# Kernel tuning notes

Measured on AMD Instinct MI355X. Metric: run time of the kernel, lower is better.

The kernel has to match this reference:

```python
import jax, jax.numpy as jnp
import numpy as np

V = 4          # view_num
B = 2048       # batch_size
D = 512        # feature dim
N = V * B
TEMP = 0.5     # temperature
EPS = 1e-8     # torch CosineSimilarity eps


def _neg_idx():
    # Row with residue p (position within its view block) masks out columns c
    # with c % B == p (the positive/self positions), exactly matching
    # mask_positive_samples: fill_diagonal_(0) on every BxB block.
    cols = np.arange(N)
    return np.stack([cols[cols % B != p] for p in range(B)])  # [B, N-V]

_NEG_IDX = jnp.asarray(_neg_idx())


def setup_inputs() -> dict:
    key = jax.random.key(0)
    x = jax.random.normal(key, (V, B, D), dtype=jnp.float32)
    return {"x": x}


def reference(x):
    # torch.cat(input, dim=0) -> [N, D]
    xf = x.reshape(N, D)
    # Cosine similarity via normalize + matmul (same math as broadcasted
    # CosineSimilarity(dim=2), expressed efficiently).
    norm = jnp.maximum(jnp.linalg.norm(xf, axis=1, keepdims=True), EPS)
    xn = xf / norm
    sim = (xn @ xn.T) / TEMP                                  # [N, N]

    # Negatives per anchor row: gather masked columns (same column order as
    # torch boolean-mask indexing, which is row-major ascending).
    sim_v = sim.reshape(V, B, N)
    negs = jnp.take_along_axis(sim_v, _NEG_IDX[None], axis=2)  # [V, B, N-V]
    lse_neg = jax.nn.logsumexp(negs, axis=2)                   # [V, B]

    # pos[i, j, b] = sim block-diagonal between views i and j
    pos = jnp.diagonal(sim.reshape(V, B, V, B), axis1=1, axis2=3)  # [V, V, B]

    # CrossEntropy with label 0 on logits = [pos_ij, negatives_i]:
    #   loss_b = logsumexp([pos, negs]) - pos = logaddexp(pos, lse_neg) - pos
    lse = jnp.logaddexp(pos, lse_neg[:, None, :])              # [V, V, B]
    per_pair = (lse - pos).sum(axis=2) / B                     # [V, V]

    off_diag = 1.0 - jnp.eye(V, dtype=per_pair.dtype)          # skip j == i
    return jnp.sum(per_pair * off_diag)
```

## Files before the change

kernel.cpp:

```cpp
#include <hip/hip_runtime.h>
#include <hip/hip_fp8.h>

#define NV 4
#define NB 2048
#define ND 512
#define NN 8192

typedef int int8v __attribute__((ext_vector_type(8)));
typedef int int4v __attribute__((ext_vector_type(4)));
typedef float floatx4 __attribute__((ext_vector_type(4)));
#define SCALE1 0x7F7F7F7Fu

__global__ __launch_bounds__(256) void normalize_k(const float* __restrict__ x,
                                                   unsigned char* __restrict__ xn,
                                                   float* __restrict__ sumexp,
                                                   float* __restrict__ out) {
  if (threadIdx.x < 4) sumexp[blockIdx.x * 4 + threadIdx.x] = 0.0f;
  if (blockIdx.x == 0 && threadIdx.x == 0) out[0] = 0.0f;

  const int row = blockIdx.x * 4 + (threadIdx.x >> 6);
  const int l = threadIdx.x & 63;
  const float4* xr = (const float4*)(x + (size_t)row * ND);
  float4 v0 = xr[l * 2 + 0];
  float4 v1 = xr[l * 2 + 1];
  float ss = v0.x * v0.x + v0.y * v0.y + v0.z * v0.z + v0.w * v0.w +
             v1.x * v1.x + v1.y * v1.y + v1.z * v1.z + v1.w * v1.w;
#pragma unroll
  for (int off = 32; off > 0; off >>= 1) ss += __shfl_xor(ss, off, 64);
  const float inv = 1.0f / fmaxf(sqrtf(ss), 1e-8f);
  union { unsigned char b[8]; uint2 u; } pk;
  pk.b[0] = __hip_fp8_e4m3(v0.x * inv).__x;
  pk.b[1] = __hip_fp8_e4m3(v0.y * inv).__x;
  pk.b[2] = __hip_fp8_e4m3(v0.z * inv).__x;
  pk.b[3] = __hip_fp8_e4m3(v0.w * inv).__x;
  pk.b[4] = __hip_fp8_e4m3(v1.x * inv).__x;
  pk.b[5] = __hip_fp8_e4m3(v1.y * inv).__x;
  pk.b[6] = __hip_fp8_e4m3(v1.z * inv).__x;
  pk.b[7] = __hip_fp8_e4m3(v1.w * inv).__x;
  *(uint2*)(xn + (size_t)row * ND + l * 8) = pk.u;
}

__global__ __launch_bounds__(512, 2) void sim_k(const unsigned char* __restrict__ xn,
                                                float* __restrict__ sumexp,
                                                float* __restrict__ pos) {
  __shared__ unsigned char As[2 * 256 * 128];
  __shared__ unsigned char Bs[2 * 256 * 128];
  const int tid = threadIdx.x;
  const int l = tid & 63;
  const int m = l & 15, q = l >> 4, s = l & 7;
  const int wid = tid >> 6;
  const int wr = wid >> 2, wc = wid & 3;

  const int bid = blockIdx.x;
  int rt = (int)((65.0f - sqrtf(4225.0f - 8.0f * (float)bid)) * 0.5f);
  rt = rt < 0 ? 0 : (rt > 31 ? 31 : rt);
  while (rt > 0 && (rt * (65 - rt) / 2) > bid) --rt;
  while (rt < 31 && ((rt + 1) * (64 - rt) / 2) <= bid) ++rt;
  const int ct = rt + (bid - rt * (65 - rt) / 2);
  const bool diag = (rt == ct);

  floatx4 acc[8][4] = {};

  const unsigned char* gA = xn + (size_t)rt * 256 * ND;
  const unsigned char* gB = xn + (size_t)ct * 256 * ND;

  const int crow = tid >> 3;
  const int coff = (tid & 7) * 16;
  const int lsw = ((tid & 7) ^ ((tid >> 3) & 7)) * 16;

  const int fo0 = ((2 * q + 0) ^ s) * 16;
  const int fo1 = ((2 * q + 1) ^ s) * 16;

  int4v pA[4], pB[4];
#pragma unroll
  for (int i = 0; i < 4; ++i) {
    const size_t go = (size_t)(i * 64 + crow) * ND + coff;
    pA[i] = *(const int4v*)(gA + go);
    pB[i] = *(const int4v*)(gB + go);
  }

#pragma unroll 1
  for (int kt = 0; kt < 4; ++kt) {
    unsigned char* Ab = As + (kt & 1) * (256 * 128);
    unsigned char* Bb = Bs + (kt & 1) * (256 * 128);
#pragma unroll
    for (int i = 0; i < 4; ++i) {
      const int la = (i * 64 + crow) * 128 + lsw;
      *(int4v*)(Ab + la) = pA[i];
      *(int4v*)(Bb + la) = pB[i];
    }
    __syncthreads();
    if (kt < 3) {
      const int kb = (kt + 1) * 128;
#pragma unroll
      for (int i = 0; i < 4; ++i) {
        const size_t go = (size_t)(i * 64 + crow) * ND + kb + coff;
        pA[i] = *(const int4v*)(gA + go);
        pB[i] = *(const int4v*)(gB + go);
      }
    }
    int8v bf0, bf1, bf2, bf3;
    {
      const unsigned char* pb0 = Bb + (wc * 64 + 0 * 16 + m) * 128;
      const unsigned char* pb1 = Bb + (wc * 64 + 1 * 16 + m) * 128;
      const unsigned char* pb2 = Bb + (wc * 64 + 2 * 16 + m) * 128;
      const unsigned char* pb3 = Bb + (wc * 64 + 3 * 16 + m) * 128;
      bf0 = __builtin_shufflevector(*(const int4v*)(pb0 + fo0),
                                    *(const int4v*)(pb0 + fo1), 0,1,2,3,4,5,6,7);
      bf1 = __builtin_shufflevector(*(const int4v*)(pb1 + fo0),
                                    *(const int4v*)(pb1 + fo1), 0,1,2,3,4,5,6,7);
      bf2 = __builtin_shufflevector(*(const int4v*)(pb2 + fo0),
                                    *(const int4v*)(pb2 + fo1), 0,1,2,3,4,5,6,7);
      bf3 = __builtin_shufflevector(*(const int4v*)(pb3 + fo0),
                                    *(const int4v*)(pb3 + fo1), 0,1,2,3,4,5,6,7);
    }
    __builtin_amdgcn_s_setprio(1);
#pragma unroll
    for (int mt = 0; mt < 8; ++mt) {
      const unsigned char* pa = Ab + (wr * 128 + mt * 16 + m) * 128;
      const int8v af = __builtin_shufflevector(*(const int4v*)(pa + fo0),
                                               *(const int4v*)(pa + fo1),
                                               0,1,2,3,4,5,6,7);
      acc[mt][0] = __builtin_amdgcn_mfma_scale_f32_16x16x128_f8f6f4(
          af, bf0, acc[mt][0], 0, 0, 0, SCALE1, 0, SCALE1);
      acc[mt][1] = __builtin_amdgcn_mfma_scale_f32_16x16x128_f8f6f4(
          af, bf1, acc[mt][1], 0, 0, 0, SCALE1, 0, SCALE1);
      acc[mt][2] = __builtin_amdgcn_mfma_scale_f32_16x16x128_f8f6f4(
          af, bf2, acc[mt][2], 0, 0, 0, SCALE1, 0, SCALE1);
      acc[mt][3] = __builtin_amdgcn_mfma_scale_f32_16x16x128_f8f6f4(
          af, bf3, acc[mt][3], 0, 0, 0, SCALE1, 0, SCALE1);
    }
    __builtin_amdgcn_s_setprio(0);
  }

  const int r0 = rt * 256 + wr * 128;
  const int c0 = ct * 256 + wc * 64;
  float cs[4] = {0.f, 0.f, 0.f, 0.f};
#pragma unroll
  for (int mt = 0; mt < 8; ++mt) {
    float rs[4] = {0.f, 0.f, 0.f, 0.f};
#pragma unroll
    for (int nt = 0; nt < 4; ++nt) {
      const int c = c0 + nt * 16 + m;
#pragma unroll
      for (int reg = 0; reg < 4; ++reg) {
        const int r = r0 + mt * 16 + q * 4 + reg;
        const float sv = acc[mt][nt][reg] * 2.0f;
        if (((c - r) & (NB - 1)) == 0) {
          pos[r * NV + (c >> 11)] = sv;
          if (!diag) pos[c * NV + (r >> 11)] = sv;
        } else {
          const float e = __expf(sv);
          rs[reg] += e;
          cs[nt] += e;
        }
      }
    }
#pragma unroll
    for (int off = 1; off < 16; off <<= 1) {
#pragma unroll
      for (int reg = 0; reg < 4; ++reg) rs[reg] += __shfl_xor(rs[reg], off, 64);
    }
    if (m < 4) atomicAdd(&sumexp[r0 + mt * 16 + q * 4 + m], rs[m]);
  }
  if (!diag) {
#pragma unroll
    for (int nt = 0; nt < 4; ++nt) {
      cs[nt] += __shfl_xor(cs[nt], 16, 64);
      cs[nt] += __shfl_xor(cs[nt], 32, 64);
    }
    if (q == 0) {
#pragma unroll
      for (int nt = 0; nt < 4; ++nt)
        atomicAdd(&sumexp[c0 + nt * 16 + m], cs[nt]);
    }
  }
}

__global__ __launch_bounds__(256) void finalize_k(
    const float* __restrict__ sumexp, const float* __restrict__ pos,
    float* __restrict__ out) {
  const int r = blockIdx.x * 256 + threadIdx.x;
  const float se = sumexp[r];
  const int i = r >> 11;
  float local = 0.0f;
#pragma unroll
  for (int j = 0; j < NV; ++j) {
    if (j == i) continue;
    const float p = pos[r * NV + j];
    local += logf(__expf(p) + se) - p;
  }
  local *= (1.0f / NB);
#pragma unroll
  for (int off = 32; off > 0; off >>= 1) local += __shfl_xor(local, off, 64);
  if ((threadIdx.x & 63) == 0) atomicAdd(out, local);
}

extern "C" void kernel_launch(void* const* d_in, const int* in_sizes, int n_in,
                              void* d_out, int out_size, void* d_ws,
                              size_t ws_size, hipStream_t stream) {
  const float* x = (const float*)d_in[0];
  float* out = (float*)d_out;
  char* ws = (char*)d_ws;
  unsigned char* xn = (unsigned char*)ws;
  float* sumexp = (float*)(ws + (size_t)NN * ND);
  float* pos = (float*)(ws + (size_t)NN * ND + NN * 4);

  normalize_k<<<NN / 4, 256, 0, stream>>>(x, xn, sumexp, out);
  sim_k<<<32 * 33 / 2, 512, 0, stream>>>(xn, sumexp, pos);
  finalize_k<<<NN / 256, 256, 0, stream>>>(sumexp, pos, out);
}
```

Measured before the change: 113.2 us.

## Stream tiles with direct global-to-LDS loads in a split-phase MFMA pipeline

Replaces the register-staged global loads and LDS stores with global_load_lds DMA into swizzled shared memory. Each K step is split into two half-tile MFMA phases, and loads for later stages are issued between them under explicit vmcnt/lgkmcnt waits and raw barriers. It also remaps block IDs so consecutive blocks spread across the triangular tile order, which may help L2 locality across XCDs. The intent is to free VGPRs and overlap memory traffic with compute. The cost is fragile manual synchronization: the slot reuse of A half 0 for stage t+2 relies on exact wait counts.

```diff
diff --git a/kernel.cpp b/kernel.cpp
--- a/kernel.cpp
+++ b/kernel.cpp
@@ -43,15 +43,19 @@
 __global__ __launch_bounds__(512, 2) void sim_k(const unsigned char* __restrict__ xn,
                                                 float* __restrict__ sumexp,
                                                 float* __restrict__ pos) {
-  __shared__ unsigned char As[2 * 256 * 128];
-  __shared__ unsigned char Bs[2 * 256 * 128];
+#define TS (256 * 128)
+  __shared__ unsigned char As[2 * TS];
+  __shared__ unsigned char Bs[2 * TS];
   const int tid = threadIdx.x;
   const int l = tid & 63;
   const int m = l & 15, q = l >> 4, s = l & 7;
-  const int wid = tid >> 6;
-  const int wr = wid >> 2, wc = wid & 3;
-
-  const int bid = blockIdx.x;
+  const int w = tid >> 6;
+  const int wr = w >> 2, wc = w & 3;
+  const int w8 = w * 8;
+  const int l8 = l >> 3;
+  const int csw = ((l & 7) ^ l8) * 16;
+
+  const int bid = (blockIdx.x & 7) * 66 + (blockIdx.x >> 3);
   int rt = (int)((65.0f - sqrtf(4225.0f - 8.0f * (float)bid)) * 0.5f);
   rt = rt < 0 ? 0 : (rt > 31 ? 31 : rt);
   while (rt > 0 && (rt * (65 - rt) / 2) > bid) --rt;
@@ -64,73 +68,101 @@
   const unsigned char* gA = xn + (size_t)rt * 256 * ND;
   const unsigned char* gB = xn + (size_t)ct * 256 * ND;
 
-  const int crow = tid >> 3;
-  const int coff = (tid & 7) * 16;
-  const int lsw = ((tid & 7) ^ ((tid >> 3) & 7)) * 16;
-
   const int fo0 = ((2 * q + 0) ^ s) * 16;
   const int fo1 = ((2 * q + 1) ^ s) * 16;
 
-  int4v pA[4], pB[4];
-#pragma unroll
-  for (int i = 0; i < 4; ++i) {
-    const size_t go = (size_t)(i * 64 + crow) * ND + coff;
-    pA[i] = *(const int4v*)(gA + go);
-    pB[i] = *(const int4v*)(gB + go);
-  }
-
-#pragma unroll 1
-  for (int kt = 0; kt < 4; ++kt) {
-    unsigned char* Ab = As + (kt & 1) * (256 * 128);
-    unsigned char* Bb = Bs + (kt & 1) * (256 * 128);
-#pragma unroll
-    for (int i = 0; i < 4; ++i) {
-      const int la = (i * 64 + crow) * 128 + lsw;
-      *(int4v*)(Ab + la) = pA[i];
-      *(int4v*)(Bb + la) = pB[i];
-    }
-    __syncthreads();
-    if (kt < 3) {
-      const int kb = (kt + 1) * 128;
-#pragma unroll
-      for (int i = 0; i < 4; ++i) {
-        const size_t go = (size_t)(i * 64 + crow) * ND + kb + coff;
-        pA[i] = *(const int4v*)(gA + go);
-        pB[i] = *(const int4v*)(gB + go);
-      }
-    }
-    int8v bf0, bf1, bf2, bf3;
-    {
-      const unsigned char* pb0 = Bb + (wc * 64 + 0 * 16 + m) * 128;
-      const unsigned char* pb1 = Bb + (wc * 64 + 1 * 16 + m) * 128;
-      const unsigned char* pb2 = Bb + (wc * 64 + 2 * 16 + m) * 128;
-      const unsigned char* pb3 = Bb + (wc * 64 + 3 * 16 + m) * 128;
-      bf0 = __builtin_shufflevector(*(const int4v*)(pb0 + fo0),
-                                    *(const int4v*)(pb0 + fo1), 0,1,2,3,4,5,6,7);
-      bf1 = __builtin_shufflevector(*(const int4v*)(pb1 + fo0),
-                                    *(const int4v*)(pb1 + fo1), 0,1,2,3,4,5,6,7);
-      bf2 = __builtin_shufflevector(*(const int4v*)(pb2 + fo0),
-                                    *(const int4v*)(pb2 + fo1), 0,1,2,3,4,5,6,7);
-      bf3 = __builtin_shufflevector(*(const int4v*)(pb3 + fo0),
-                                    *(const int4v*)(pb3 + fo1), 0,1,2,3,4,5,6,7);
-    }
+#define SBAR() __builtin_amdgcn_s_barrier()
+#define LGKM0() asm volatile("s_waitcnt lgkmcnt(0)" ::: "memory")
+#define VMW2() asm volatile("s_waitcnt vmcnt(2)" ::: "memory")
+#define VMW0() asm volatile("s_waitcnt vmcnt(0)" ::: "memory")
+
+#define GLL16(gp, lp)                                                        \
+  __builtin_amdgcn_global_load_lds(                                          \
+      (const __attribute__((address_space(1))) void*)(gp),                   \
+      (__attribute__((address_space(3))) void*)(lp), 16, 0, 0)
+
+#define STAGE_A(slot_, mh_, kt_)                                             \
+  do {                                                                       \
+    GLL16(gA + (size_t)((mh_) * 64 + w8 + l8) * ND + (kt_) * 128 + csw,      \
+          As + (slot_) * TS + ((mh_) * 64 + w8) * 128);                      \
+    GLL16(gA + (size_t)(128 + (mh_) * 64 + w8 + l8) * ND + (kt_) * 128 + csw,\
+          As + (slot_) * TS + (128 + (mh_) * 64 + w8) * 128);                \
+  } while (0)
+#define STAGE_B(slot_, h_, kt_)                                              \
+  do {                                                                       \
+    GLL16(gB + (size_t)((h_) * 128 + w8 + l8) * ND + (kt_) * 128 + csw,      \
+          Bs + (slot_) * TS + ((h_) * 128 + w8) * 128);                      \
+    GLL16(gB + (size_t)((h_) * 128 + 64 + w8 + l8) * ND + (kt_) * 128 + csw, \
+          Bs + (slot_) * TS + ((h_) * 128 + 64 + w8) * 128);                 \
+  } while (0)
+
+#define LDFRAG(dst, base, row)                                               \
+  do {                                                                       \
+    const unsigned char* p_ = (base) + (size_t)(row) * 128;                  \
+    dst = __builtin_shufflevector(*(const int4v*)(p_ + fo0),                 \
+                                  *(const int4v*)(p_ + fo1),                 \
+                                  0, 1, 2, 3, 4, 5, 6, 7);                   \
+  } while (0)
+
+#define MFMA4(mt, afv)                                                       \
+  acc[mt][0] = __builtin_amdgcn_mfma_scale_f32_16x16x128_f8f6f4(             \
+      afv, bf0, acc[mt][0], 0, 0, 0, SCALE1, 0, SCALE1);                     \
+  acc[mt][1] = __builtin_amdgcn_mfma_scale_f32_16x16x128_f8f6f4(             \
+      afv, bf1, acc[mt][1], 0, 0, 0, SCALE1, 0, SCALE1);                     \
+  acc[mt][2] = __builtin_amdgcn_mfma_scale_f32_16x16x128_f8f6f4(             \
+      afv, bf2, acc[mt][2], 0, 0, 0, SCALE1, 0, SCALE1);                     \
+  acc[mt][3] = __builtin_amdgcn_mfma_scale_f32_16x16x128_f8f6f4(             \
+      afv, bf3, acc[mt][3], 0, 0, 0, SCALE1, 0, SCALE1)
+
+  STAGE_A(0, 0, 0);
+  STAGE_A(0, 1, 0);
+  STAGE_B(0, 0, 0);
+  STAGE_B(0, 1, 0);
+  STAGE_A(1, 0, 1);
+  VMW2();
+  SBAR();
+
+#pragma unroll
+  for (int t = 0; t < 4; ++t) {
+    const unsigned char* Asl = As + (t & 1) * TS;
+    const unsigned char* Bsl = Bs + (t & 1) * TS;
+    const int os = (t & 1) ^ 1;
+    int8v af0, af1, af2, af3, bf0, bf1, bf2, bf3;
+    LDFRAG(af0, Asl, wr * 128 + 0 * 16 + m);
+    LDFRAG(af1, Asl, wr * 128 + 1 * 16 + m);
+    LDFRAG(af2, Asl, wr * 128 + 2 * 16 + m);
+    LDFRAG(af3, Asl, wr * 128 + 3 * 16 + m);
+    LDFRAG(bf0, Bsl, wc * 64 + 0 * 16 + m);
+    LDFRAG(bf1, Bsl, wc * 64 + 1 * 16 + m);
+    LDFRAG(bf2, Bsl, wc * 64 + 2 * 16 + m);
+    LDFRAG(bf3, Bsl, wc * 64 + 3 * 16 + m);
+    if (t < 3) { STAGE_A(os, 1, t + 1); STAGE_B(os, 0, t + 1); }
+    SBAR();
+    LGKM0();
     __builtin_amdgcn_s_setprio(1);
-#pragma unroll
-    for (int mt = 0; mt < 8; ++mt) {
-      const unsigned char* pa = Ab + (wr * 128 + mt * 16 + m) * 128;
-      const int8v af = __builtin_shufflevector(*(const int4v*)(pa + fo0),
-                                               *(const int4v*)(pa + fo1),
-                                               0,1,2,3,4,5,6,7);
-      acc[mt][0] = __builtin_amdgcn_mfma_scale_f32_16x16x128_f8f6f4(
-          af, bf0, acc[mt][0], 0, 0, 0, SCALE1, 0, SCALE1);
-      acc[mt][1] = __builtin_amdgcn_mfma_scale_f32_16x16x128_f8f6f4(
-          af, bf1, acc[mt][1], 0, 0, 0, SCALE1, 0, SCALE1);
-      acc[mt][2] = __builtin_amdgcn_mfma_scale_f32_16x16x128_f8f6f4(
-          af, bf2, acc[mt][2], 0, 0, 0, SCALE1, 0, SCALE1);
-      acc[mt][3] = __builtin_amdgcn_mfma_scale_f32_16x16x128_f8f6f4(
-          af, bf3, acc[mt][3], 0, 0, 0, SCALE1, 0, SCALE1);
-    }
+    MFMA4(0, af0);
+    MFMA4(1, af1);
+    MFMA4(2, af2);
+    MFMA4(3, af3);
     __builtin_amdgcn_s_setprio(0);
+    SBAR();
+    LDFRAG(af0, Asl, wr * 128 + 64 + 0 * 16 + m);
+    LDFRAG(af1, Asl, wr * 128 + 64 + 1 * 16 + m);
+    LDFRAG(af2, Asl, wr * 128 + 64 + 2 * 16 + m);
+    LDFRAG(af3, Asl, wr * 128 + 64 + 3 * 16 + m);
+    if (t < 3) STAGE_B(os, 1, t + 1);
+    if (t < 2) STAGE_A(t & 1, 0, t + 2);
+    SBAR();
+    LGKM0();
+    __builtin_amdgcn_s_setprio(1);
+    MFMA4(4, af0);
+    MFMA4(5, af1);
+    MFMA4(6, af2);
+    MFMA4(7, af3);
+    __builtin_amdgcn_s_setprio(0);
+    if (t < 2) VMW2();
+    else if (t == 2) VMW0();
+    SBAR();
   }
 
   const int r0 = rt * 256 + wr * 128;
```

Measured after the change: 278.1 us. 146% more time.
